# Kernel optimization log

Measured on AMD Instinct MI355X. Metric: run time of the kernel, lower is better.

The kernel has to match this reference:

```python
import jax, jax.numpy as jnp
import numpy as np

E, T, D = 100000, 400000, 128
LN_EPS = 1e-5


def setup_inputs() -> dict:
    key = jax.random.key(0)
    k1, k2, k3 = jax.random.split(key, 3)
    f_edge = jax.random.normal(k1, (E, D), dtype=jnp.float32)
    W = jax.random.normal(k2, (3 * D, D), dtype=jnp.float32) / np.sqrt(3 * D)
    b = jnp.zeros((D,), dtype=jnp.float32)
    gamma = jnp.ones((D,), dtype=jnp.float32)
    beta = jnp.zeros((D,), dtype=jnp.float32)
    triangle = jax.random.randint(k3, (T, 3), 0, E, dtype=jnp.int64)
    return {"f_edge": f_edge, "W": W, "b": b, "gamma": gamma, "beta": beta,
            "triangle": triangle}


def reference(f_edge, W, b, gamma, beta, triangle):
    # f_edge [E, D], triangle [T, 3] -> gather to [T, 3, D], flatten to [T, 3D]
    t = triangle.shape[0]
    e, d = f_edge.shape
    f_tri = f_edge[triangle].reshape(t, 3 * d)
    # Linear(3D -> D) + exact GELU (torch nn.GELU default is erf-based)
    h = jax.nn.gelu(f_tri @ W + b, approximate=False)  # [T, D]
    # scatter_mean over destination edge index triangle[:, 2], dim_size=E
    dst = triangle[:, 2]
    seg_sum = jax.ops.segment_sum(h, dst, num_segments=e)            # [E, D]
    cnt = jax.ops.segment_sum(jnp.ones((t,), h.dtype), dst, num_segments=e)
    mean = seg_sum / jnp.maximum(cnt, 1.0)[:, None]
    # dropout is identity in eval mode; LayerNorm over last dim
    mu = jnp.mean(mean, axis=-1, keepdims=True)
    var = jnp.mean(jnp.square(mean - mu), axis=-1, keepdims=True)
    return (mean - mu) / jnp.sqrt(var + LN_EPS) * gamma + beta
```

## Files before the change

kernel.cpp:

```cpp
#include <hip/hip_runtime.h>
#include <hip/hip_bf16.h>

typedef __attribute__((ext_vector_type(8))) short short8;
typedef __attribute__((ext_vector_type(4))) float floatx4;
typedef __attribute__((ext_vector_type(4))) unsigned int uintx4;

__device__ __forceinline__ float gelu_fast(float x)
{
    float u = 0.7978845608f * x * (1.0f + 0.044715f * x * x);
    float e = __builtin_amdgcn_exp2f(2.885390082f * u);
    return x - x * __builtin_amdgcn_rcpf(e + 1.0f);
}

__global__ __launch_bounds__(256)
void prep(const float* __restrict__ Wg, uintx4* __restrict__ wq,
          const int* __restrict__ tri, int* __restrict__ cnt,
          int* __restrict__ slot, int T)
{
    int g = blockIdx.x * 256 + threadIdx.x;
    if (g < T) {
        int i2 = tri[g * 3 + 2];
        slot[g] = atomicAdd(&cnt[i2], 1);
    } else {
        int i = g - T;
        if (i < 6144) {
            int frag = i >> 6, lane = i & 63;
            int ko = frag >> 3, nt = frag & 7;
            int col = lane & 15, quad = lane >> 4;
            unsigned short tmp[8] __attribute__((aligned(16)));
#pragma unroll
            for (int j = 0; j < 8; ++j) {
                __hip_bfloat16 b =
                    __float2bfloat16(Wg[(ko * 32 + quad * 8 + j) * 128 + nt * 16 + col]);
                tmp[j] = *(unsigned short*)&b;
            }
            wq[i] = *(const uintx4*)tmp;
        }
    }
}

__device__ __forceinline__ int wave_incl_scan(int v, int lane)
{
#pragma unroll
    for (int o = 1; o < 64; o <<= 1) {
        int u = __shfl_up(v, o);
        if (lane >= o) v += u;
    }
    return v;
}

__global__ __launch_bounds__(1024)
void scan_blk(const int* __restrict__ in, int* __restrict__ outExcl,
              int* __restrict__ partial, int n)
{
    __shared__ int ws[16];
    int t = threadIdx.x;
    int g = blockIdx.x * 1024 + t;
    int lane = t & 63, wv = t >> 6;
    int v = (g < n) ? in[g] : 0;
    int sc = wave_incl_scan(v, lane);
    if (lane == 63) ws[wv] = sc;
    __syncthreads();
    if (wv == 0) {
        int b = (lane < 16) ? ws[lane] : 0;
        int bs = wave_incl_scan(b, lane);
        if (lane < 16) ws[lane] = bs;
    }
    __syncthreads();
    int off = wv ? ws[wv - 1] : 0;
    if (g < n) outExcl[g] = off + sc - v;
    if (partial && t == 0) partial[blockIdx.x] = ws[15];
}

__global__ __launch_bounds__(256)
void scatter(const int* __restrict__ tri, const int* __restrict__ slot,
             const int* __restrict__ excl, const int* __restrict__ pscan,
             const int* __restrict__ cnt, int2* __restrict__ srec,
             int2* __restrict__ rowinfo, int E, int T)
{
    int g = blockIdx.x * 256 + threadIdx.x;
    if (g < T) {
        int i0 = tri[g * 3 + 0];
        int i1 = tri[g * 3 + 1];
        int i2 = tri[g * 3 + 2];
        int pos = excl[i2] + pscan[i2 >> 10] + slot[g];
        srec[pos] = make_int2(i0 << 8, i1 << 8);
    }
    if (g < E)
        rowinfo[g] = make_int2(excl[g] + pscan[g >> 10], cnt[g]);
    if (g < 8)
        srec[T + g] = make_int2(0, 0);
}

__global__ __launch_bounds__(1024, 1)
void edge_gemm(const float* __restrict__ fe_f, const uintx4* __restrict__ wq,
               unsigned short* __restrict__ G, int E)
{
    __shared__ uintx4 ldsW[6144];

    const int tid  = threadIdx.x;
    const int wv   = tid >> 6;
    const int lane = tid & 63;
    const int col  = lane & 15;
    const int quad = lane >> 4;
    const int ntiles = (E + 15) >> 4;

    for (int i = tid; i < 6144; i += 1024) ldsW[i] = wq[i];
    __syncthreads();

#pragma unroll 1
    for (int tile = blockIdx.x * 16 + wv; tile < ntiles; tile += gridDim.x * 16) {
        int row_a = tile * 16 + col;
        if (row_a >= E) row_a = E - 1;
        const float* arow = fe_f + (size_t)row_a * 128 + quad * 8;

        floatx4 f[8];
#pragma unroll
        for (int l = 0; l < 8; ++l)
            f[l] = *(const floatx4*)(arow + (l >> 1) * 32 + (l & 1) * 4);

        short8 a[4];
#pragma unroll
        for (int ko = 0; ko < 4; ++ko) {
            unsigned short tmp[8] __attribute__((aligned(16)));
#pragma unroll
            for (int j = 0; j < 8; ++j) {
                __hip_bfloat16 b = __float2bfloat16(f[ko * 2 + (j >> 2)][j & 3]);
                tmp[j] = *(unsigned short*)&b;
            }
            a[ko] = *(const short8*)tmp;
        }

#pragma unroll 1
        for (int r = 0; r < 3; ++r) {
            floatx4 acc[8];
#pragma unroll
            for (int nt = 0; nt < 8; ++nt) acc[nt] = (floatx4)0.0f;

#pragma unroll
            for (int ko = 0; ko < 4; ++ko) {
#pragma unroll
                for (int nt = 0; nt < 8; ++nt) {
                    short8 bf = *(const short8*)&ldsW[r * 2048 + (ko * 8 + nt) * 64 + lane];
                    acc[nt] = __builtin_amdgcn_mfma_f32_16x16x32_bf16(a[ko], bf, acc[nt], 0, 0, 0);
                }
            }

            unsigned short* Gr = G + (size_t)r * E * 128;
#pragma unroll
            for (int rr = 0; rr < 4; ++rr) {
                int row = tile * 16 + quad * 4 + rr;
                if (row < E) {
                    unsigned short pk[8] __attribute__((aligned(16)));
#pragma unroll
                    for (int nt = 0; nt < 8; ++nt) {
                        __hip_bfloat16 hb = __float2bfloat16(acc[nt][rr]);
                        pk[nt] = *(unsigned short*)&hb;
                    }
                    *(uintx4*)(Gr + (size_t)row * 128 + col * 8) = *(const uintx4*)pk;
                }
            }
        }
    }
}

__global__ __launch_bounds__(256)
void mean_ln(const unsigned short* __restrict__ G, const int2* __restrict__ rowinfo,
             const int2* __restrict__ srec, const float* __restrict__ bias,
             const float* __restrict__ gamma, const float* __restrict__ beta,
             float* __restrict__ out, int E)
{
    const int tid  = threadIdx.x;
    const int lane = tid & 63;
    const int wid  = tid >> 6;
    const int h    = lane >> 4;
    const int s    = lane & 15;

    const char* g0 = (const char*)G + s * 16;
    const char* g1 = g0 + (size_t)E * 256;
    const char* g2 = g1 + (size_t)E * 256;

    float bv[8], gm[8], bt[8];
#pragma unroll
    for (int k = 0; k < 8; ++k) {
        bv[k] = bias[k * 16 + s];
        gm[k] = gamma[k * 16 + s];
        bt[k] = beta[k * 16 + s];
    }

    const int ngroups = (E + 3) >> 2;
    const int nwaves  = gridDim.x * 4;

    for (int grp = blockIdx.x * 4 + wid; grp < ngroups; grp += nwaves) {
        int row  = grp * 4 + h;
        int rowc = row < E ? row : E - 1;

        int2 ri = rowinfo[rowc];
        int start = ri.x, c = ri.y;

        int cmax = max(c, __shfl_xor(c, 16));
        cmax = max(cmax, __shfl_xor(cmax, 32));

        uintx4 w2 = *(const uintx4*)(g2 + (size_t)rowc * 256);
        float base[8];
#pragma unroll
        for (int k = 0; k < 8; ++k) {
            unsigned int wv = (k & 1) ? (w2[k >> 1] & 0xffff0000u)
                                      : (w2[k >> 1] << 16);
            base[k] = __uint_as_float(wv) + bv[k];
        }

        float x[8];
#pragma unroll
        for (int k = 0; k < 8; ++k) x[k] = 0.0f;

        for (int t = 0; t < cmax; t += 4) {
            int ci = t + (s & 3);
            int cl = c - 1; if (cl < 0) cl = 0;
            if (ci > cl) ci = cl;
            int2 rr = srec[start + ci];
#pragma unroll
            for (int k = 0; k < 4; ++k) {
                unsigned int o0 = (unsigned)__shfl(rr.x, (h << 4) + k);
                unsigned int o1 = (unsigned)__shfl(rr.y, (h << 4) + k);
                uintx4 a = *(const uintx4*)(g0 + (size_t)o0);
                uintx4 b = *(const uintx4*)(g1 + (size_t)o1);
                bool ok = (t + k) < c;
#pragma unroll
                for (int p = 0; p < 8; ++p) {
                    unsigned int wa = (p & 1) ? (a[p >> 1] & 0xffff0000u)
                                              : (a[p >> 1] << 16);
                    unsigned int wb = (p & 1) ? (b[p >> 1] & 0xffff0000u)
                                              : (b[p >> 1] << 16);
                    float sv = __uint_as_float(wa) + __uint_as_float(wb) + base[p];
                    x[p] += ok ? gelu_fast(sv) : 0.0f;
                }
            }
        }

        float inv = 1.0f / fmaxf((float)c, 1.0f);
        float sm = 0.0f;
#pragma unroll
        for (int k = 0; k < 8; ++k) { x[k] *= inv; sm += x[k]; }
#pragma unroll
        for (int o = 8; o > 0; o >>= 1) sm += __shfl_xor(sm, o);
        float mu = sm * (1.0f / 128.0f);
        float vv = 0.0f;
#pragma unroll
        for (int k = 0; k < 8; ++k) { x[k] -= mu; vv += x[k] * x[k]; }
#pragma unroll
        for (int o = 8; o > 0; o >>= 1) vv += __shfl_xor(vv, o);
        float rstd = rsqrtf(vv * (1.0f / 128.0f) + 1e-5f);

        if (row < E) {
            float* orow = out + (size_t)row * 128 + s;
#pragma unroll
            for (int k = 0; k < 8; ++k)
                __builtin_nontemporal_store(x[k] * rstd * gm[k] + bt[k],
                                            &orow[k * 16]);
        }
    }
}

extern "C" void kernel_launch(void* const* d_in, const int* in_sizes, int n_in,
                              void* d_out, int out_size, void* d_ws, size_t ws_size,
                              hipStream_t stream)
{
    const float* fe_f  = (const float*)d_in[0];
    const float* Wg    = (const float*)d_in[1];
    const float* bias  = (const float*)d_in[2];
    const float* gamma = (const float*)d_in[3];
    const float* beta  = (const float*)d_in[4];
    const int*   tri   = (const int*)d_in[5];

    int E = in_sizes[0] / 128;
    int T = in_sizes[5] / 3;

    unsigned short* G = (unsigned short*)d_ws;
    int2* srec = (int2*)((char*)d_ws + (size_t)3 * E * 256);
    uintx4* wq = (uintx4*)(srec + T + 8);
    int* slot = (int*)(wq + 6144);
    int* cnt  = slot + T;
    int* excl = cnt + E;
    int* partial = excl + E;
    int* pscan = partial + 1024;
    int2* rowinfo = (int2*)(pscan + 1024);

    (void)hipMemsetAsync(cnt, 0, (size_t)E * sizeof(int), stream);

    int total = T + 6144;
    prep<<<(total + 255) / 256, 256, 0, stream>>>(Wg, wq, tri, cnt, slot, T);

    int NB = (E + 1023) / 1024;
    scan_blk<<<NB, 1024, 0, stream>>>(cnt, excl, partial, E);
    scan_blk<<<1, 1024, 0, stream>>>(partial, pscan, nullptr, NB);

    scatter<<<(T + 255) / 256, 256, 0, stream>>>(tri, slot, excl, pscan, cnt,
                                                 srec, rowinfo, E, T);

    edge_gemm<<<256, 1024, 0, stream>>>(fe_f, wq, G, E);

    mean_ln<<<2048, 256, 0, stream>>>(G, rowinfo, srec, bias, gamma, beta,
                                      (float*)d_out, E);
}
```

Measured before the change: 215.7 us.

## Sort edge rows by triangle count to balance mean_ln wave work

Builds a histogram of per-edge counts during the block scan and converts it to prefix offsets. The scatter kernel then counting-sorts edges into a rank-ordered sinfo array that packs start and count. mean_ln processes rows in that order, so the four rows in each wave have similar counts and less work is lost to the cmax divergence. The cost is extra global atomics on 64 histogram bins, scattered output writes, and counts of 255 or more needing a fallback read from cnt.

Result: slower. 608.0 us (+181.8%).

```diff
diff --git a/kernel.cpp b/kernel.cpp
--- a/kernel.cpp
+++ b/kernel.cpp
@@ -51,32 +51,43 @@
 
 __global__ __launch_bounds__(1024)
 void scan_blk(const int* __restrict__ in, int* __restrict__ outExcl,
-              int* __restrict__ partial, int n)
+              int* __restrict__ partial, int n,
+              int* __restrict__ hist, int* __restrict__ histx)
 {
     __shared__ int ws[16];
+    __shared__ int lh[64];
     int t = threadIdx.x;
     int g = blockIdx.x * 1024 + t;
     int lane = t & 63, wv = t >> 6;
     int v = (g < n) ? in[g] : 0;
     int sc = wave_incl_scan(v, lane);
     if (lane == 63) ws[wv] = sc;
+    if (hist && !histx && t < 64) lh[t] = 0;
     __syncthreads();
     if (wv == 0) {
         int b = (lane < 16) ? ws[lane] : 0;
         int bs = wave_incl_scan(b, lane);
         if (lane < 16) ws[lane] = bs;
     }
+    if (hist && !histx && g < n) atomicAdd(&lh[v < 63 ? v : 63], 1);
     __syncthreads();
     int off = wv ? ws[wv - 1] : 0;
     if (g < n) outExcl[g] = off + sc - v;
     if (partial && t == 0) partial[blockIdx.x] = ws[15];
+    if (hist && !histx && t < 64 && lh[t]) atomicAdd(&hist[t], lh[t]);
+    if (histx && t < 64) {
+        int hv = hist[t];
+        int hs = wave_incl_scan(hv, lane);
+        histx[t] = hs - hv;
+    }
 }
 
 __global__ __launch_bounds__(256)
 void scatter(const int* __restrict__ tri, const int* __restrict__ slot,
              const int* __restrict__ excl, const int* __restrict__ pscan,
              const int* __restrict__ cnt, int2* __restrict__ srec,
-             int2* __restrict__ rowinfo, int E, int T)
+             const int* __restrict__ histx, int* __restrict__ histcur,
+             int2* __restrict__ sinfo, int E, int T)
 {
     int g = blockIdx.x * 256 + threadIdx.x;
     if (g < T) {
@@ -86,8 +97,13 @@
         int pos = excl[i2] + pscan[i2 >> 10] + slot[g];
         srec[pos] = make_int2(i0 << 8, i1 << 8);
     }
-    if (g < E)
-        rowinfo[g] = make_int2(excl[g] + pscan[g >> 10], cnt[g]);
+    if (g < E) {
+        int c = cnt[g];
+        int start = excl[g] + pscan[g >> 10];
+        int cc = c < 63 ? c : 63;
+        int rank = histx[cc] + atomicAdd(&histcur[cc], 1);
+        sinfo[rank] = make_int2((start << 8) | (c < 255 ? c : 255), g);
+    }
     if (g < 8)
         srec[T + g] = make_int2(0, 0);
 }
@@ -165,10 +181,10 @@
 }
 
 __global__ __launch_bounds__(256)
-void mean_ln(const unsigned short* __restrict__ G, const int2* __restrict__ rowinfo,
-             const int2* __restrict__ srec, const float* __restrict__ bias,
-             const float* __restrict__ gamma, const float* __restrict__ beta,
-             float* __restrict__ out, int E)
+void mean_ln(const unsigned short* __restrict__ G, const int2* __restrict__ sinfo,
+             const int* __restrict__ cnt, const int2* __restrict__ srec,
+             const float* __restrict__ bias, const float* __restrict__ gamma,
+             const float* __restrict__ beta, float* __restrict__ out, int E)
 {
     const int tid  = threadIdx.x;
     const int lane = tid & 63;
@@ -192,16 +208,19 @@
     const int nwaves  = gridDim.x * 4;
 
     for (int grp = blockIdx.x * 4 + wid; grp < ngroups; grp += nwaves) {
-        int row  = grp * 4 + h;
-        int rowc = row < E ? row : E - 1;
-
-        int2 ri = rowinfo[rowc];
-        int start = ri.x, c = ri.y;
+        int rank = grp * 4 + h;
+        int rk   = rank < E ? rank : E - 1;
+
+        int2 si  = sinfo[rk];
+        int row  = si.y;
+        int c    = si.x & 255;
+        int start = (int)((unsigned)si.x >> 8);
+        if (__builtin_expect(c == 255, 0)) c = cnt[row];
 
         int cmax = max(c, __shfl_xor(c, 16));
         cmax = max(cmax, __shfl_xor(cmax, 32));
 
-        uintx4 w2 = *(const uintx4*)(g2 + (size_t)rowc * 256);
+        uintx4 w2 = *(const uintx4*)(g2 + (size_t)row * 256);
         float base[8];
 #pragma unroll
         for (int k = 0; k < 8; ++k) {
@@ -214,9 +233,9 @@
 #pragma unroll
         for (int k = 0; k < 8; ++k) x[k] = 0.0f;
 
+        int cl = c - 1; if (cl < 0) cl = 0;
         for (int t = 0; t < cmax; t += 4) {
             int ci = t + (s & 3);
-            int cl = c - 1; if (cl < 0) cl = 0;
             if (ci > cl) ci = cl;
             int2 rr = srec[start + ci];
 #pragma unroll
@@ -252,7 +271,7 @@
         for (int o = 8; o > 0; o >>= 1) vv += __shfl_xor(vv, o);
         float rstd = rsqrtf(vv * (1.0f / 128.0f) + 1e-5f);
 
-        if (row < E) {
+        if (rank < E) {
             float* orow = out + (size_t)row * 128 + s;
 #pragma unroll
             for (int k = 0; k < 8; ++k)
@@ -281,25 +300,30 @@
     uintx4* wq = (uintx4*)(srec + T + 8);
     int* slot = (int*)(wq + 6144);
     int* cnt  = slot + T;
-    int* excl = cnt + E;
+    int* hist = cnt + E;
+    int* histcur = hist + 64;
+    int* histx = histcur + 64;
+    int* excl = histx + 64;
     int* partial = excl + E;
     int* pscan = partial + 1024;
-    int2* rowinfo = (int2*)(pscan + 1024);
-
-    (void)hipMemsetAsync(cnt, 0, (size_t)E * sizeof(int), stream);
+    int2* sinfo = (int2*)(pscan + 1024);
+
+    (void)hipMemsetAsync(cnt, 0, (size_t)E * sizeof(int) + 128 * sizeof(int),
+                         stream);
 
     int total = T + 6144;
     prep<<<(total + 255) / 256, 256, 0, stream>>>(Wg, wq, tri, cnt, slot, T);
 
     int NB = (E + 1023) / 1024;
-    scan_blk<<<NB, 1024, 0, stream>>>(cnt, excl, partial, E);
-    scan_blk<<<1, 1024, 0, stream>>>(partial, pscan, nullptr, NB);
+    scan_blk<<<NB, 1024, 0, stream>>>(cnt, excl, partial, E, hist, nullptr);
+    scan_blk<<<1, 1024, 0, stream>>>(partial, pscan, nullptr, NB, hist, histx);
 
     scatter<<<(T + 255) / 256, 256, 0, stream>>>(tri, slot, excl, pscan, cnt,
-                                                 srec, rowinfo, E, T);
+                                                 srec, histx, histcur, sinfo,
+                                                 E, T);
 
     edge_gemm<<<256, 1024, 0, stream>>>(fe_f, wq, G, E);
 
-    mean_ln<<<2048, 256, 0, stream>>>(G, rowinfo, srec, bias, gamma, beta,
+    mean_ln<<<2048, 256, 0, stream>>>(G, sinfo, cnt, srec, bias, gamma, beta,
                                       (float*)d_out, E);
 }
```
